# Optimization experiments

Measured on AMD Instinct MI355X. Metric: run time of the kernel, lower is better.

The kernel has to match this reference:

```python
import jax, jax.numpy as jnp
import numpy as np

NUM_HEADS = 16
BLOCK_SIZE = 64


def setup_inputs() -> dict:
    key = jax.random.key(0)
    ks = jax.random.split(key, 5)
    B, S, C = 2, 2047, 1024
    return {
        "x": jax.random.normal(ks[0], (B, S, C), dtype=jnp.float32),
        "global_token": jax.random.normal(ks[1], (1, 1, C), dtype=jnp.float32),
        "qkv_w": jax.random.normal(ks[2], (3 * C, C), dtype=jnp.float32) * 0.02,
        "proj_w": jax.random.normal(ks[3], (C, C), dtype=jnp.float32) * 0.02,
        "proj_b": jax.random.normal(ks[4], (C,), dtype=jnp.float32) * 0.02,
    }


def reference(x, global_token, qkv_w, proj_w, proj_b):
    B, S, C = x.shape
    H = NUM_HEADS
    D = C // H
    scale = D ** -0.5
    # prepend global token -> N = S + 1
    g = jnp.broadcast_to(global_token, (B, 1, C))
    xg = jnp.concatenate([g, x], axis=1)
    N = S + 1
    # fused qkv projection (torch Linear: x @ W^T)
    qkv = (xg @ qkv_w.T).reshape(B, N, 3, H, D)
    qkv = jnp.transpose(qkv, (2, 0, 3, 1, 4))  # [3, B, H, N, D]
    q, k, v = qkv[0], qkv[1], qkv[2]
    # block-causal mask: query t sees key j iff block(j) <= block(t)
    blk = jnp.arange(N) // BLOCK_SIZE
    mask = blk[:, None] >= blk[None, :]  # [N, N]
    attn = jnp.einsum("bhqd,bhkd->bhqk", q, k) * scale
    attn = jnp.where(mask[None, None], attn, -jnp.inf)
    attn = jax.nn.softmax(attn, axis=-1)
    out = jnp.einsum("bhqk,bhkd->bhqd", attn, v)
    out = jnp.transpose(out, (0, 2, 1, 3)).reshape(B, N, C)
    out = out[:, 1:, :]  # drop global token
    return out @ proj_w.T + proj_b
```

## Files before the change

kernel.cpp:

```cpp
#include <hip/hip_runtime.h>
#include <math.h>

typedef _Float16 h16;
typedef _Float16 half8 __attribute__((ext_vector_type(8)));
typedef _Float16 half4 __attribute__((ext_vector_type(4)));
typedef float f32x4 __attribute__((ext_vector_type(4)));

#define NB 2
#define NS 2047
#define NC 1024
#define NN 2048
#define NH 16
#define ND 64

__device__ __forceinline__ void gl_lds16(const h16* g, h16* l) {
  __builtin_amdgcn_global_load_lds((const __attribute__((address_space(1))) void*)g,
                                   (__attribute__((address_space(3))) void*)l, 16, 0, 0);
}
__device__ __forceinline__ f32x4 mfma32(half8 a, half8 b, f32x4 c) {
  return __builtin_amdgcn_mfma_f32_16x16x32_f16(a, b, c, 0, 0, 0);
}
__device__ __forceinline__ f32x4 mfma16x(half4 a, half4 b, f32x4 c) {
  return __builtin_amdgcn_mfma_f32_16x16x16f16(a, b, c, 0, 0, 0);
}

__global__ __launch_bounds__(256) void cast_all_k(
    const float* __restrict__ x, const float* __restrict__ g,
    const float* __restrict__ qw, const float* __restrict__ pw, h16* __restrict__ out) {
  const size_t i = ((size_t)blockIdx.x * 256 + threadIdx.x) * 8;
  const float* src;
  if (i < (size_t)NB * NN * NC) {
    const int c = (int)(i & (NC - 1));
    const int n = (int)((i >> 10) & (NN - 1));
    const int b = (int)(i >> 21);
    src = (n == 0) ? (g + c) : (x + ((size_t)b * NS + (n - 1)) * NC + c);
  } else {
    const size_t j = i - (size_t)NB * NN * NC;
    src = (j < (size_t)3 * NC * NC) ? (qw + j) : (pw + (j - (size_t)3 * NC * NC));
  }
  float4 f0 = ((const float4*)src)[0];
  float4 f1 = ((const float4*)src)[1];
  h16 tmp[8];
  tmp[0] = (h16)f0.x; tmp[1] = (h16)f0.y; tmp[2] = (h16)f0.z; tmp[3] = (h16)f0.w;
  tmp[4] = (h16)f1.x; tmp[5] = (h16)f1.y; tmp[6] = (h16)f1.z; tmp[7] = (h16)f1.w;
  *(half8*)(out + i) = *(half8*)&tmp[0];
}

__global__ __launch_bounds__(512, 2) void gemm_qkv_h(
    const h16* __restrict__ A, const h16* __restrict__ W,
    h16* __restrict__ qP, h16* __restrict__ kP, h16* __restrict__ vP) {
  __shared__ h16 SM[32768];
  const int tid = threadIdx.x;
  const int flat = blockIdx.y * 12 + blockIdx.x;
  const int swz = (flat & 7) * 24 + (flat >> 3);
  const int m0 = (swz / 12) * 256, j0 = (swz % 12) * 256;
  const int wid = tid >> 6, lane = tid & 63, l15 = lane & 15, quad = lane >> 4;
  const int wm = wid >> 2, wn = wid & 3;

  const int glin = (lane & 7) ^ (lane >> 3);
  const int rowoff = glin >> 2, kg = glin & 3;
  const int srow = (wid * 8 + (lane >> 3)) * 2 + rowoff;
  const h16* ag = A + (size_t)(m0 + srow) * NC + kg * 8;
  const h16* bg = W + (size_t)(j0 + srow) * NC + kg * 8;

  const int rsw = l15 >> 1;
  const int gs = (((l15 & 1) << 2) | quad) ^ rsw;
  const int aoff = wm * 4096 + rsw * 64 + gs * 8;
  const int boff = wn * 2048 + rsw * 64 + gs * 8;

  f32x4 acc[8][4];
#pragma unroll
  for (int fm = 0; fm < 8; ++fm)
#pragma unroll
    for (int fn = 0; fn < 4; ++fn) acc[fm][fn] = (f32x4){0.f, 0.f, 0.f, 0.f};

  gl_lds16(ag, &SM[(wid * 8) * 64]);
  gl_lds16(ag + (size_t)128 * NC, &SM[(64 + wid * 8) * 64]);
  gl_lds16(bg, &SM[16384 + (wid * 8) * 64]);
  gl_lds16(bg + (size_t)128 * NC, &SM[16384 + (64 + wid * 8) * 64]);

  for (int kt = 0; kt < 32; ++kt) {
    const int cur = kt & 1, nxt = cur ^ 1;
    const int k1 = (kt + 1) * 32;
    const bool pre = (kt < 31);
    const h16* Ab = SM + cur * 8192;
    const h16* Bb = SM + 16384 + cur * 8192;

    if (pre) {
      gl_lds16(ag + k1, &SM[nxt * 8192 + (wid * 8) * 64]);
      gl_lds16(ag + (size_t)128 * NC + k1, &SM[nxt * 8192 + (64 + wid * 8) * 64]);
      asm volatile("s_waitcnt vmcnt(2)" ::: "memory");
    } else {
      asm volatile("s_waitcnt vmcnt(0)" ::: "memory");
    }
    asm volatile("s_barrier" ::: "memory");

    half8 bf[4];
#pragma unroll
    for (int fn = 0; fn < 4; ++fn) bf[fn] = *(const half8*)&Bb[boff + fn * 512];

#pragma unroll
    for (int q = 0; q < 4; ++q) {
      if (q == 1 && pre)
        gl_lds16(bg + k1, &SM[16384 + nxt * 8192 + (wid * 8) * 64]);
      if (q == 2 && pre)
        gl_lds16(bg + (size_t)128 * NC + k1, &SM[16384 + nxt * 8192 + (64 + wid * 8) * 64]);
      half8 af0 = *(const half8*)&Ab[aoff + (q * 2 + 0) * 512];
      half8 af1 = *(const half8*)&Ab[aoff + (q * 2 + 1) * 512];
      __builtin_amdgcn_s_setprio(1);
#pragma unroll
      for (int fn = 0; fn < 4; ++fn) {
        acc[q * 2 + 0][fn] = mfma32(af0, bf[fn], acc[q * 2 + 0][fn]);
        acc[q * 2 + 1][fn] = mfma32(af1, bf[fn], acc[q * 2 + 1][fn]);
      }
      __builtin_amdgcn_s_setprio(0);
    }
    asm volatile("s_barrier" ::: "memory");
  }

  const int b = m0 >> 11, n0 = m0 & (NN - 1);
  if (j0 < 2 * NC) {
    h16* base = (j0 < NC) ? qP : kP;
    const int coff = (j0 < NC) ? 0 : NC;
    const int h = (j0 - coff + wn * 64) >> 6;
    h16* dst = base + ((size_t)(b * NH + h) * NN + n0) * ND;
#pragma unroll
    for (int fm = 0; fm < 8; ++fm)
#pragma unroll
      for (int fn = 0; fn < 4; ++fn)
#pragma unroll
        for (int r = 0; r < 4; ++r) {
          const int mloc = wm * 128 + fm * 16 + quad * 4 + r;
          dst[(size_t)mloc * ND + fn * 16 + l15] = (h16)acc[fm][fn][r];
        }
  } else {
    const int kb0 = n0 >> 6;
    const int h0 = (j0 - 2 * NC) >> 6;
    const int g = tid >> 6, d = tid & 63;
    __syncthreads();
#pragma unroll
    for (int p = 0; p < 2; ++p) {
      if (p) __syncthreads();
      if (wm == p) {
#pragma unroll
        for (int fm = 0; fm < 8; ++fm)
#pragma unroll
          for (int fn = 0; fn < 4; ++fn)
#pragma unroll
            for (int r = 0; r < 4; ++r) {
              const int lrow = fm * 16 + quad * 4 + r;
              const int col = wn * 64 + fn * 16 + l15;
              SM[lrow * 256 + (col ^ ((lrow & 7) << 3))] = (h16)acc[fm][fn][r];
            }
      }
      __syncthreads();
#pragma unroll
      for (int u = 0; u < 4; ++u) {
        const int idx = g * 4 + u;
        const int kbl2 = idx >> 4, hl = (idx >> 2) & 3, w4 = idx & 3;
        const int bh = b * NH + h0 + hl;
        h16 buf[16];
#pragma unroll
        for (int kk = 0; kk < 16; ++kk) {
          const int lrow = kbl2 * 64 + w4 * 16 + kk;
          buf[kk] = SM[lrow * 256 + ((hl * 64 + d) ^ ((lrow & 7) << 3))];
        }
        h16* dstv = vP + ((size_t)((bh * 32 + kb0 + p * 2 + kbl2) * 4 + w4)) * 1024 + d * 16;
        *(half8*)dstv = *(half8*)&buf[0];
        *(half8*)(dstv + 8) = *(half8*)&buf[8];
      }
    }
  }
}

__global__ __launch_bounds__(256, 3) void attn_h(
    const h16* __restrict__ qP, const h16* __restrict__ kP,
    const h16* __restrict__ vP, h16* __restrict__ outp) {
  __shared__ float RED[2 * 64 * 36];
  __shared__ float DEN[4 * 64];
  const int bx = blockIdx.x;
  const int qb = 31 - (bx >> 5);
  const int bh = bx & 31;
  const int b = bh >> 4, h = bh & 15;
  const int tid = threadIdx.x, w = tid >> 6, lane = tid & 63;
  const int l15 = lane & 15, quad = lane >> 4;

  half8 bq[4][2];
#pragma unroll
  for (int nt = 0; nt < 4; ++nt) {
    const h16* qp = qP + ((size_t)bh * NN + qb * 64 + nt * 16 + l15) * ND + quad * 8;
    bq[nt][0] = (*(const half8*)qp) * (h16)0.125f;
    bq[nt][1] = (*(const half8*)(qp + 32)) * (h16)0.125f;
  }
  const h16* kbase = kP + ((size_t)bh * NN + w * 16 + l15) * ND + quad * 8;
  const h16* vbase = vP + ((size_t)bh * 32 * 4 + w) * 1024 + l15 * 16 + quad * 4;

  f32x4 o[4][4];
  float den[4] = {0.f, 0.f, 0.f, 0.f};
#pragma unroll
  for (int mt = 0; mt < 4; ++mt)
#pragma unroll
    for (int nt = 0; nt < 4; ++nt) o[mt][nt] = (f32x4){0.f, 0.f, 0.f, 0.f};

  half8 kf0 = *(const half8*)kbase;
  half8 kf1 = *(const half8*)(kbase + 32);
  half4 vf0 = *(const half4*)(vbase);
  half4 vf1 = *(const half4*)(vbase + 256);
  half4 vf2 = *(const half4*)(vbase + 512);
  half4 vf3 = *(const half4*)(vbase + 768);

  for (int kb = 0; kb <= qb; ++kb) {
    const int nkb = (kb < qb) ? kb + 1 : kb;
    const h16* kn = kbase + (size_t)nkb * 64 * ND;
    const h16* vn = vbase + (size_t)nkb * 4096;
    half8 nk0 = *(const half8*)kn;
    half8 nk1 = *(const half8*)(kn + 32);
    half4 nv0 = *(const half4*)(vn);
    half4 nv1 = *(const half4*)(vn + 256);
    half4 nv2 = *(const half4*)(vn + 512);
    half4 nv3 = *(const half4*)(vn + 768);
    __builtin_amdgcn_s_setprio(1);
#pragma unroll
    for (int nt = 0; nt < 4; ++nt) {
      f32x4 s = (f32x4){0.f, 0.f, 0.f, 0.f};
      s = mfma32(kf0, bq[nt][0], s);
      s = mfma32(kf1, bq[nt][1], s);
      float e0 = __expf(s[0]), e1 = __expf(s[1]);
      float e2 = __expf(s[2]), e3 = __expf(s[3]);
      den[nt] += (e0 + e1) + (e2 + e3);
      int2 pi;
      pi.x = __builtin_bit_cast(int, __builtin_amdgcn_cvt_pkrtz(e0, e1));
      pi.y = __builtin_bit_cast(int, __builtin_amdgcn_cvt_pkrtz(e2, e3));
      half4 p = __builtin_bit_cast(half4, pi);
      o[0][nt] = mfma16x(vf0, p, o[0][nt]);
      o[1][nt] = mfma16x(vf1, p, o[1][nt]);
      o[2][nt] = mfma16x(vf2, p, o[2][nt]);
      o[3][nt] = mfma16x(vf3, p, o[3][nt]);
    }
    __builtin_amdgcn_s_setprio(0);
    kf0 = nk0; kf1 = nk1;
    vf0 = nv0; vf1 = nv1; vf2 = nv2; vf3 = nv3;
  }

#pragma unroll
  for (int nt = 0; nt < 4; ++nt) {
    den[nt] += __shfl_xor(den[nt], 16);
    den[nt] += __shfl_xor(den[nt], 32);
  }
  __syncthreads();
  if (quad == 0) {
#pragma unroll
    for (int nt = 0; nt < 4; ++nt) DEN[w * 64 + nt * 16 + l15] = den[nt];
  }
#pragma unroll
  for (int r = 0; r < 2; ++r) {
    if (r) __syncthreads();
    if (w < 2) {
#pragma unroll
      for (int mt2 = 0; mt2 < 2; ++mt2)
#pragma unroll
        for (int nt = 0; nt < 4; ++nt)
          *(f32x4*)&RED[(w * 64 + nt * 16 + l15) * 36 + mt2 * 16 + quad * 4] =
              o[r * 2 + mt2][nt];
    }
    __syncthreads();
    if (w >= 2) {
#pragma unroll
      for (int mt2 = 0; mt2 < 2; ++mt2)
#pragma unroll
        for (int nt = 0; nt < 4; ++nt) {
          float* p = &RED[((w - 2) * 64 + nt * 16 + l15) * 36 + mt2 * 16 + quad * 4];
          f32x4 t = *(f32x4*)p;
          *(f32x4*)p = t + o[r * 2 + mt2][nt];
        }
    }
    __syncthreads();
    {
      const int q = w * 16 + l15;
      const float dt = DEN[q] + DEN[64 + q] + DEN[128 + q] + DEN[192 + q];
      const float inv = 1.f / dt;
      f32x4 x0 = *(const f32x4*)&RED[(0 * 64 + q) * 36 + quad * 8];
      f32x4 x1 = *(const f32x4*)&RED[(0 * 64 + q) * 36 + quad * 8 + 4];
      f32x4 y0 = *(const f32x4*)&RED[(1 * 64 + q) * 36 + quad * 8];
      f32x4 y1 = *(const f32x4*)&RED[(1 * 64 + q) * 36 + quad * 8 + 4];
      x0 += y0;
      x1 += y1;
      int4 pk;
      pk.x = __builtin_bit_cast(int, __builtin_amdgcn_cvt_pkrtz(x0[0] * inv, x0[1] * inv));
      pk.y = __builtin_bit_cast(int, __builtin_amdgcn_cvt_pkrtz(x0[2] * inv, x0[3] * inv));
      pk.z = __builtin_bit_cast(int, __builtin_amdgcn_cvt_pkrtz(x1[0] * inv, x1[1] * inv));
      pk.w = __builtin_bit_cast(int, __builtin_amdgcn_cvt_pkrtz(x1[2] * inv, x1[3] * inv));
      h16* op = outp + (size_t)(b * NN + qb * 64 + q) * NC + h * ND + r * 32 + quad * 8;
      *(half8*)op = __builtin_bit_cast(half8, pk);
    }
  }
}

__global__ __launch_bounds__(256) void gemm_proj_h(
    const h16* __restrict__ Ah, const h16* __restrict__ W,
    const float* __restrict__ bias, float* __restrict__ out) {
  __shared__ h16 As[64 * 64];
  __shared__ h16 Bs[128 * 64];
  const int tid = threadIdx.x;
  const int flat = blockIdx.y * 8 + blockIdx.x;
  const int swz = (flat & 7) * 64 + (flat >> 3);
  const int m0 = (swz >> 3) * 64, j0 = (swz & 7) * 128;
  const int wid = tid >> 6, lane = tid & 63, l15 = lane & 15, quad = lane >> 4;
  const int wr = wid >> 1, wc = wid & 1;
  const int rl = lane >> 3, csw = (lane & 7) ^ rl;
  const h16* ag[2];
#pragma unroll
  for (int i = 0; i < 2; ++i) {
    int m = m0 + wid * 16 + i * 8 + rl;
    if (m > NB * NS - 1) m = NB * NS - 1;
    const int bb = (m >= NS) ? 1 : 0;
    ag[i] = Ah + (size_t)(bb * NN + m - bb * NS + 1) * NC + csw * 8;
  }
  const h16* bg = W + (size_t)(j0 + wid * 32 + rl) * NC + csw * 8;
  f32x4 acc[2][4];
#pragma unroll
  for (int rt = 0; rt < 2; ++rt)
#pragma unroll
    for (int ct = 0; ct < 4; ++ct) acc[rt][ct] = (f32x4){0.f, 0.f, 0.f, 0.f};

  for (int k0 = 0; k0 < NC; k0 += 64) {
    __syncthreads();
    gl_lds16(ag[0] + k0, &As[(wid * 16) * 64]);
    gl_lds16(ag[1] + k0, &As[(wid * 16 + 8) * 64]);
#pragma unroll
    for (int i = 0; i < 4; ++i)
      gl_lds16(bg + (size_t)i * 8 * NC + k0, &Bs[(wid * 32 + i * 8) * 64]);
    __syncthreads();
#pragma unroll
    for (int ks = 0; ks < 2; ++ks) {
      const int p0 = ((ks * 4 + quad) ^ (l15 & 7)) * 8;
      half8 af[2], bf[4];
#pragma unroll
      for (int rt = 0; rt < 2; ++rt)
        af[rt] = *(const half8*)&As[(wr * 32 + rt * 16 + l15) * 64 + p0];
#pragma unroll
      for (int ct = 0; ct < 4; ++ct)
        bf[ct] = *(const half8*)&Bs[(wc * 64 + ct * 16 + l15) * 64 + p0];
#pragma unroll
      for (int rt = 0; rt < 2; ++rt)
#pragma unroll
        for (int ct = 0; ct < 4; ++ct)
          acc[rt][ct] = mfma32(af[rt], bf[ct], acc[rt][ct]);
    }
  }
#pragma unroll
  for (int ct = 0; ct < 4; ++ct) {
    const float bv = bias[j0 + wc * 64 + ct * 16 + l15];
#pragma unroll
    for (int rt = 0; rt < 2; ++rt)
#pragma unroll
      for (int r = 0; r < 4; ++r) {
        const int mm = m0 + wr * 32 + rt * 16 + quad * 4 + r;
        if (mm < NB * NS)
          out[(size_t)mm * NC + j0 + wc * 64 + ct * 16 + l15] = acc[rt][ct][r] + bv;
      }
  }
}

extern "C" void kernel_launch(void* const* d_in, const int* in_sizes, int n_in,
                              void* d_out, int out_size, void* d_ws, size_t ws_size,
                              hipStream_t stream) {
  const float* x = (const float*)d_in[0];
  const float* g = (const float*)d_in[1];
  const float* qkv_w = (const float*)d_in[2];
  const float* proj_w = (const float*)d_in[3];
  const float* proj_b = (const float*)d_in[4];
  float* out = (float*)d_out;

  h16* xgh  = (h16*)d_ws;
  h16* w3h  = xgh + (size_t)NB * NN * NC;
  h16* wph  = w3h + (size_t)3 * NC * NC;
  h16* qP   = wph + (size_t)NC * NC;
  h16* kP   = qP + (size_t)NB * NH * NN * ND;
  h16* vP   = kP + (size_t)NB * NH * NN * ND;
  h16* attnh = vP + (size_t)NB * NH * NN * ND;

  cast_all_k<<<dim3(4096), 256, 0, stream>>>(x, g, qkv_w, proj_w, xgh);
  gemm_qkv_h<<<dim3(12, 16), 512, 0, stream>>>(xgh, w3h, qP, kP, vP);
  attn_h<<<dim3(1024), 256, 0, stream>>>(qP, kP, vP, attnh);
  gemm_proj_h<<<dim3(8, 64), 256, 0, stream>>>(attnh, wph, proj_b, out);
}
```

Measured before the change: 170.9 us.

## Double-buffer proj GEMM with 128x128 tiles, 512 threads and async LDS prefetch

Rewrites the output projection GEMM to use 128x128 tiles with 8 waves, a K step of 32, and double-buffered LDS. The next tile is fetched through global_load_lds while the current one runs MFMAs, with manual vmcnt waits and raw s_barriers in place of two __syncthreads per step. It also raises wave priority around the MFMAs. This aims to hide load latency and improve data reuse, but the grid drops to 256 blocks, which may reduce occupancy and parallelism on a GPU with many CUs.

```diff
diff --git a/kernel.cpp b/kernel.cpp
--- a/kernel.cpp
+++ b/kernel.cpp
@@ -296,68 +296,82 @@
   }
 }
 
-__global__ __launch_bounds__(256) void gemm_proj_h(
+__global__ __launch_bounds__(512) void gemm_proj_h(
     const h16* __restrict__ Ah, const h16* __restrict__ W,
     const float* __restrict__ bias, float* __restrict__ out) {
-  __shared__ h16 As[64 * 64];
-  __shared__ h16 Bs[128 * 64];
+  __shared__ h16 SM[16384];
   const int tid = threadIdx.x;
   const int flat = blockIdx.y * 8 + blockIdx.x;
-  const int swz = (flat & 7) * 64 + (flat >> 3);
-  const int m0 = (swz >> 3) * 64, j0 = (swz & 7) * 128;
+  const int swz = (flat & 7) * 32 + (flat >> 3);
+  const int m0 = (swz >> 3) * 128, j0 = (swz & 7) * 128;
   const int wid = tid >> 6, lane = tid & 63, l15 = lane & 15, quad = lane >> 4;
-  const int wr = wid >> 1, wc = wid & 1;
-  const int rl = lane >> 3, csw = (lane & 7) ^ rl;
-  const h16* ag[2];
-#pragma unroll
-  for (int i = 0; i < 2; ++i) {
-    int m = m0 + wid * 16 + i * 8 + rl;
-    if (m > NB * NS - 1) m = NB * NS - 1;
-    const int bb = (m >= NS) ? 1 : 0;
-    ag[i] = Ah + (size_t)(bb * NN + m - bb * NS + 1) * NC + csw * 8;
-  }
-  const h16* bg = W + (size_t)(j0 + wid * 32 + rl) * NC + csw * 8;
-  f32x4 acc[2][4];
-#pragma unroll
-  for (int rt = 0; rt < 2; ++rt)
-#pragma unroll
-    for (int ct = 0; ct < 4; ++ct) acc[rt][ct] = (f32x4){0.f, 0.f, 0.f, 0.f};
-
-  for (int k0 = 0; k0 < NC; k0 += 64) {
-    __syncthreads();
-    gl_lds16(ag[0] + k0, &As[(wid * 16) * 64]);
-    gl_lds16(ag[1] + k0, &As[(wid * 16 + 8) * 64]);
-#pragma unroll
-    for (int i = 0; i < 4; ++i)
-      gl_lds16(bg + (size_t)i * 8 * NC + k0, &Bs[(wid * 32 + i * 8) * 64]);
-    __syncthreads();
-#pragma unroll
-    for (int ks = 0; ks < 2; ++ks) {
-      const int p0 = ((ks * 4 + quad) ^ (l15 & 7)) * 8;
-      half8 af[2], bf[4];
-#pragma unroll
-      for (int rt = 0; rt < 2; ++rt)
-        af[rt] = *(const half8*)&As[(wr * 32 + rt * 16 + l15) * 64 + p0];
-#pragma unroll
-      for (int ct = 0; ct < 4; ++ct)
-        bf[ct] = *(const half8*)&Bs[(wc * 64 + ct * 16 + l15) * 64 + p0];
-#pragma unroll
-      for (int rt = 0; rt < 2; ++rt)
-#pragma unroll
-        for (int ct = 0; ct < 4; ++ct)
-          acc[rt][ct] = mfma32(af[rt], bf[ct], acc[rt][ct]);
-    }
-  }
-#pragma unroll
-  for (int ct = 0; ct < 4; ++ct) {
-    const float bv = bias[j0 + wc * 64 + ct * 16 + l15];
-#pragma unroll
-    for (int rt = 0; rt < 2; ++rt)
+  const int wm = wid >> 2, wn = wid & 3;
+
+  const int glin = (lane & 7) ^ (lane >> 3);
+  const int rowoff = glin >> 2, kg = glin & 3;
+  const int srow = (wid * 8 + (lane >> 3)) * 2 + rowoff;
+  int m_r = m0 + srow;
+  if (m_r > NB * NS - 1) m_r = NB * NS - 1;
+  const int bb = (m_r >= NS) ? 1 : 0;
+  const h16* ag = Ah + (size_t)(bb * NN + m_r - bb * NS + 1) * NC + kg * 8;
+  const h16* bg = W + (size_t)(j0 + srow) * NC + kg * 8;
+
+  const int rsw = l15 >> 1;
+  const int gs = (((l15 & 1) << 2) | quad) ^ rsw;
+  const int aoff = wm * 2048 + rsw * 64 + gs * 8;
+  const int boff = wn * 1024 + rsw * 64 + gs * 8;
+
+  f32x4 acc[4][2];
+#pragma unroll
+  for (int fm = 0; fm < 4; ++fm)
+#pragma unroll
+    for (int fn = 0; fn < 2; ++fn) acc[fm][fn] = (f32x4){0.f, 0.f, 0.f, 0.f};
+
+  gl_lds16(ag, &SM[(wid * 8) * 64]);
+  gl_lds16(bg, &SM[8192 + (wid * 8) * 64]);
+
+  for (int kt = 0; kt < 32; ++kt) {
+    const int cur = kt & 1, nxt = cur ^ 1;
+    const int k1 = (kt + 1) * 32;
+    const bool pre = (kt < 31);
+    const h16* Ab = SM + cur * 4096;
+    const h16* Bb = SM + 8192 + cur * 4096;
+
+    if (pre) {
+      gl_lds16(ag + k1, &SM[nxt * 4096 + (wid * 8) * 64]);
+      asm volatile("s_waitcnt vmcnt(1)" ::: "memory");
+    } else {
+      asm volatile("s_waitcnt vmcnt(0)" ::: "memory");
+    }
+    asm volatile("s_barrier" ::: "memory");
+
+    half8 bf[2];
+#pragma unroll
+    for (int fn = 0; fn < 2; ++fn) bf[fn] = *(const half8*)&Bb[boff + fn * 512];
+
+#pragma unroll
+    for (int q = 0; q < 4; ++q) {
+      if (q == 2 && pre)
+        gl_lds16(bg + k1, &SM[8192 + nxt * 4096 + (wid * 8) * 64]);
+      half8 af = *(const half8*)&Ab[aoff + q * 512];
+      __builtin_amdgcn_s_setprio(1);
+      acc[q][0] = mfma32(af, bf[0], acc[q][0]);
+      acc[q][1] = mfma32(af, bf[1], acc[q][1]);
+      __builtin_amdgcn_s_setprio(0);
+    }
+    asm volatile("s_barrier" ::: "memory");
+  }
+
+#pragma unroll
+  for (int fn = 0; fn < 2; ++fn) {
+    const int jj = j0 + wn * 32 + fn * 16 + l15;
+    const float bv = bias[jj];
+#pragma unroll
+    for (int fm = 0; fm < 4; ++fm)
 #pragma unroll
       for (int r = 0; r < 4; ++r) {
-        const int mm = m0 + wr * 32 + rt * 16 + quad * 4 + r;
-        if (mm < NB * NS)
-          out[(size_t)mm * NC + j0 + wc * 64 + ct * 16 + l15] = acc[rt][ct][r] + bv;
+        const int mm = m0 + wm * 64 + fm * 16 + quad * 4 + r;
+        if (mm < NB * NS) out[(size_t)mm * NC + jj] = acc[fm][fn][r] + bv;
       }
   }
 }
@@ -383,5 +397,5 @@
   cast_all_k<<<dim3(4096), 256, 0, stream>>>(x, g, qkv_w, proj_w, xgh);
   gemm_qkv_h<<<dim3(12, 16), 512, 0, stream>>>(xgh, w3h, qP, kP, vP);
   attn_h<<<dim3(1024), 256, 0, stream>>>(qP, kP, vP, attnh);
-  gemm_proj_h<<<dim3(8, 64), 256, 0, stream>>>(attnh, wph, proj_b, out);
-}
+  gemm_proj_h<<<dim3(8, 32), 512, 0, stream>>>(attnh, wph, proj_b, out);
+}
```

New measurement: 172.2 us. No clear change (+0.8%).
